# Optimization experiments

Hardware: AMD Instinct MI355X
Metric: run time of the kernel (lower is better)

The kernel has to match this reference:

```python
import jax, jax.numpy as jnp
import numpy as np

EMB = 512
HEADS = 8

def setup_inputs() -> dict:
    key = jax.random.key(0)
    ks = jax.random.split(key, 9)
    s = 1.0 / np.sqrt(EMB)
    return {
        'x':  jax.random.normal(ks[0], (4, 2048, EMB), dtype=jnp.float32),
        'Wq': jax.random.uniform(ks[1], (EMB, EMB), jnp.float32, -s, s),
        'bq': jax.random.uniform(ks[2], (EMB,), jnp.float32, -s, s),
        'Wk': jax.random.uniform(ks[3], (EMB, EMB), jnp.float32, -s, s),
        'bk': jax.random.uniform(ks[4], (EMB,), jnp.float32, -s, s),
        'Wv': jax.random.uniform(ks[5], (EMB, EMB), jnp.float32, -s, s),
        'bv': jax.random.uniform(ks[6], (EMB,), jnp.float32, -s, s),
        'Wo': jax.random.uniform(ks[7], (EMB, EMB), jnp.float32, -s, s),
        'bo': jax.random.uniform(ks[8], (EMB,), jnp.float32, -s, s),
    }

def reference(x, Wq, bq, Wk, bk, Wv, bv, Wo, bo):
    b, n, e = x.shape
    h = HEADS
    d = e // h
    def split_heads(t):
        return t.reshape(b, n, h, d).transpose(0, 2, 1, 3)  # b h n d
    q = split_heads(x @ Wq.T + bq)
    k = split_heads(x @ Wk.T + bk)
    v = split_heads(x @ Wv.T + bv)
    energy = jnp.einsum('bhqd,bhkd->bhqk', q, k)
    scaling = jnp.sqrt(jnp.float32(e))  # NOTE: sqrt(emb_size), not sqrt(head_dim), per source
    att = jax.nn.softmax(energy / scaling, axis=-1)
    out = jnp.einsum('bhal,bhlv->bhav', att, v)  # b h n d
    out = out.transpose(0, 2, 1, 3).reshape(b, n, e)
    return out @ Wo.T + bo
```

## Files before the change

kernel.cpp:

```cpp
#include <hip/hip_runtime.h>

typedef float f32x4 __attribute__((ext_vector_type(4)));
typedef float f32x16 __attribute__((ext_vector_type(16)));
typedef short bf16x8 __attribute__((ext_vector_type(8)));
typedef unsigned int uint;
typedef unsigned short ushort_t;

#define EMB    512
#define NSEQ   2048
#define NBATCH 4
#define NHEAD  8
#define MROWS  (NBATCH * NSEQ)
#define CEXP   0.06375872f

__device__ __forceinline__ uint f2bf(float x) {
    uint u = __builtin_bit_cast(uint, x);
    return (u + 0x7fffu + ((u >> 16) & 1u)) >> 16;
}

__device__ __forceinline__ void glds16(const void* g, void* l) {
    __builtin_amdgcn_global_load_lds(
        (const __attribute__((address_space(1))) uint*)g,
        (__attribute__((address_space(3))) uint*)l, 16, 0, 0);
}

__global__ __launch_bounds__(256)
void prep(const float* __restrict__ x,
          const float* __restrict__ Wq, const float* __restrict__ Wk,
          const float* __restrict__ Wv, const float* __restrict__ Wo,
          const float* __restrict__ bq, const float* __restrict__ bk,
          const float* __restrict__ bv,
          ushort_t* __restrict__ xb, ushort_t* __restrict__ Wqkvb,
          float* __restrict__ bqkv, ushort_t* __restrict__ Wob) {
    int t = blockIdx.x * 256 + threadIdx.x;
    {
        float4 v = ((const float4*)x)[t];
        uint2 p;
        p.x = f2bf(v.x) | (f2bf(v.y) << 16);
        p.y = f2bf(v.z) | (f2bf(v.w) << 16);
        ((uint2*)xb)[t] = p;
    }
    if (t < 65536) {
        float4 a = ((const float4*)Wq)[t];
        float4 b = ((const float4*)Wk)[t];
        float4 c = ((const float4*)Wv)[t];
        float4 d = ((const float4*)Wo)[t];
        uint2 p;
        p.x = f2bf(a.x) | (f2bf(a.y) << 16); p.y = f2bf(a.z) | (f2bf(a.w) << 16);
        ((uint2*)Wqkvb)[t] = p;
        p.x = f2bf(b.x) | (f2bf(b.y) << 16); p.y = f2bf(b.z) | (f2bf(b.w) << 16);
        ((uint2*)Wqkvb)[t + 65536] = p;
        p.x = f2bf(c.x) | (f2bf(c.y) << 16); p.y = f2bf(c.z) | (f2bf(c.w) << 16);
        ((uint2*)Wqkvb)[t + 131072] = p;
        p.x = f2bf(d.x) | (f2bf(d.y) << 16); p.y = f2bf(d.z) | (f2bf(d.w) << 16);
        ((uint2*)Wob)[t] = p;
    }
    if (t < 512) {
        bqkv[t] = bq[t]; bqkv[512 + t] = bk[t]; bqkv[1024 + t] = bv[t];
    }
}

template<int MODE>
__global__ __launch_bounds__(256)
void gemm128(const ushort_t* __restrict__ A, const ushort_t* __restrict__ BT,
             const float* __restrict__ bias, ushort_t* __restrict__ oQK,
             ushort_t* __restrict__ oVT, float* __restrict__ oC) {
    __shared__ ushort_t As[128][32];
    __shared__ ushort_t Bs[128][32];
    __shared__ float ep[32][132];
    const int tid = threadIdx.x, wave = tid >> 6, lane = tid & 63;
    const int m0 = blockIdx.x * 128, n0 = blockIdx.y * 128;
    const int wr = (wave & 1) * 64, wc = (wave >> 1) * 64;

    f32x4 acc[4][4];
#pragma unroll
    for (int i = 0; i < 4; ++i)
#pragma unroll
        for (int j = 0; j < 4; ++j) acc[i][j] = (f32x4){0.f, 0.f, 0.f, 0.f};

    const int grow = wave * 16 + (lane >> 2);
    const int gcol = (lane & 3) * 8;
    const ushort_t* Ag = A  + (size_t)(m0 + grow) * 512 + gcol;
    const ushort_t* Bg = BT + (size_t)(n0 + grow) * 512 + gcol;
    ushort_t* lA0 = &As[wave * 16][0];
    ushort_t* lA1 = &As[64 + wave * 16][0];
    ushort_t* lB0 = &Bs[wave * 16][0];
    ushort_t* lB1 = &Bs[64 + wave * 16][0];
    const int fr = lane & 15, fc = (lane >> 4) * 8;

    for (int kt = 0; kt < 16; ++kt) {
        __syncthreads();
        glds16(Ag + kt * 32,             lA0);
        glds16(Ag + kt * 32 + 64 * 512,  lA1);
        glds16(Bg + kt * 32,             lB0);
        glds16(Bg + kt * 32 + 64 * 512,  lB1);
        __syncthreads();
        bf16x8 af[4], bf[4];
#pragma unroll
        for (int i = 0; i < 4; ++i) af[i] = *(const bf16x8*)&As[wr + i * 16 + fr][fc];
#pragma unroll
        for (int j = 0; j < 4; ++j) bf[j] = *(const bf16x8*)&Bs[wc + j * 16 + fr][fc];
#pragma unroll
        for (int i = 0; i < 4; ++i)
#pragma unroll
            for (int j = 0; j < 4; ++j)
                acc[i][j] = __builtin_amdgcn_mfma_f32_16x16x32_bf16(af[i], bf[j], acc[i][j], 0, 0, 0);
    }

    const int col_l = lane & 15, row_l = (lane >> 4) * 4;

    if (MODE == 0 && n0 >= 1024) {
#pragma unroll
        for (int j = 0; j < 4; ++j) {
            const int col = n0 + wc + j * 16 + col_l;
            const float bv = bias[col];
#pragma unroll
            for (int i = 0; i < 4; ++i) {
                const int row = m0 + wr + i * 16 + row_l;
                f32x4 v = acc[i][j];
                v += (f32x4){bv, bv, bv, bv};
                const int e = col - 1024;
                const int b = row >> 11, tok = row & 2047;
                uint2 p;
                p.x = f2bf(v[0]) | (f2bf(v[1]) << 16);
                p.y = f2bf(v[2]) | (f2bf(v[3]) << 16);
                *(uint2*)&oVT[((size_t)(b * 512 + e)) * 2048 + tok] = p;
            }
        }
        return;
    }

    const float scale = (MODE == 0 && n0 < 512) ? CEXP : 1.0f;
    float bv[4];
#pragma unroll
    for (int j = 0; j < 4; ++j) bv[j] = bias[n0 + wc + j * 16 + col_l];

    const int erow = tid >> 3, eseg = (tid & 7) * 16;
#pragma unroll
    for (int c = 0; c < 4; ++c) {
        __syncthreads();
        if (wr == (c >> 1) * 64) {
#pragma unroll
            for (int ii = 0; ii < 2; ++ii) {
                const int i = (c & 1) * 2 + ii;
#pragma unroll
                for (int j = 0; j < 4; ++j) {
                    f32x4 v = acc[i][j];
#pragma unroll
                    for (int r = 0; r < 4; ++r)
                        ep[ii * 16 + row_l + r][wc + j * 16 + col_l] = (v[r] + bv[j]) * scale;
                }
            }
        }
        __syncthreads();
        const int grow2 = m0 + c * 32 + erow;
        if (MODE == 0) {
            uint4 o0, o1;
#pragma unroll
            for (int k = 0; k < 4; ++k) {
                uint lo = f2bf(ep[erow][eseg + k * 2])     | (f2bf(ep[erow][eseg + k * 2 + 1]) << 16);
                uint hi = f2bf(ep[erow][eseg + 8 + k * 2]) | (f2bf(ep[erow][eseg + 9 + k * 2]) << 16);
                ((uint*)&o0)[k] = lo; ((uint*)&o1)[k] = hi;
            }
            *(uint4*)&oQK[(size_t)grow2 * 1024 + n0 + eseg]     = o0;
            *(uint4*)&oQK[(size_t)grow2 * 1024 + n0 + eseg + 8] = o1;
        } else {
#pragma unroll
            for (int k = 0; k < 4; ++k) {
                f32x4 v = *(const f32x4*)&ep[erow][eseg + k * 4];
                *(f32x4*)&oC[(size_t)grow2 * 512 + n0 + eseg + k * 4] = v;
            }
        }
    }
}

template<int NSLICE>
__global__ __launch_bounds__(256, 4)
void attn_mfma(const ushort_t* __restrict__ QK, const ushort_t* __restrict__ VT,
               float* __restrict__ Op, float* __restrict__ Lp,
               ushort_t* __restrict__ AO) {
    __shared__ ushort_t Ks[64][72];
    __shared__ ushort_t Vs[64][72];

    const int tid = threadIdx.x, w = tid >> 6, lane = tid & 63;
    const int qt = blockIdx.x, bh = blockIdx.y, b = bh >> 3, h = bh & 7;
    const int slice = (NSLICE > 1) ? blockIdx.z : 0;
    const int l31 = lane & 31, lhi = lane >> 5;

    const int tok = qt * 128 + w * 32 + l31;
    const size_t qrow = (size_t)(b * NSEQ + tok);
    bf16x8 qf[4];
#pragma unroll
    for (int ks = 0; ks < 4; ++ks)
        qf[ks] = *(const bf16x8*)&QK[qrow * 1024 + h * 64 + ks * 16 + lhi * 8];

    f32x16 accO[2];
#pragma unroll
    for (int i = 0; i < 16; ++i) { accO[0][i] = 0.f; accO[1][i] = 0.f; }
    float lpart = 0.f;

    const int sr = tid & 63, sc = (tid >> 6) * 16;
    const ushort_t* Kg = QK + (size_t)(b * NSEQ) * 1024 + 512 + h * 64;
    const ushort_t* Vg = VT + ((size_t)(b * 512 + h * 64)) * 2048;

    const int kt0 = slice * (32 / NSLICE), kt1 = kt0 + 32 / NSLICE;
    for (int kt = kt0; kt < kt1; ++kt) {
        const int k0 = kt * 64;
        uint4 kv0 = *(const uint4*)&Kg[(size_t)(k0 + sr) * 1024 + sc];
        uint4 kv1 = *(const uint4*)&Kg[(size_t)(k0 + sr) * 1024 + sc + 8];
        uint4 vv0 = *(const uint4*)&Vg[(size_t)sr * 2048 + k0 + sc];
        uint4 vv1 = *(const uint4*)&Vg[(size_t)sr * 2048 + k0 + sc + 8];
        __syncthreads();
        *(uint4*)&Ks[sr][sc] = kv0;  *(uint4*)&Ks[sr][sc + 8] = kv1;
        *(uint4*)&Vs[sr][sc] = vv0;  *(uint4*)&Vs[sr][sc + 8] = vv1;
        __syncthreads();

#pragma unroll
        for (int ms = 0; ms < 2; ++ms) {
            f32x16 st;
#pragma unroll
            for (int i = 0; i < 16; ++i) st[i] = 0.f;
#pragma unroll
            for (int ks = 0; ks < 4; ++ks) {
                bf16x8 ka = *(const bf16x8*)&Ks[ms * 32 + l31][ks * 16 + lhi * 8];
                st = __builtin_amdgcn_mfma_f32_32x32x16_bf16(ka, qf[ks], st, 0, 0, 0);
            }
            uint dd[8], ee[8];
#pragma unroll
            for (int i = 0; i < 8; ++i) {
                uint ua = __builtin_bit_cast(uint, __builtin_amdgcn_exp2f(st[2 * i]));
                uint ub = __builtin_bit_cast(uint, __builtin_amdgcn_exp2f(st[2 * i + 1]));
                lpart += __builtin_bit_cast(float, ua & 0xffff0000u)
                       + __builtin_bit_cast(float, ub & 0xffff0000u);
                dd[i] = (ua >> 16) | (ub & 0xffff0000u);
            }
#pragma unroll
            for (int i = 0; i < 8; ++i) ee[i] = (uint)__shfl_xor((int)dd[i], 32);
#pragma unroll
            for (int s = 0; s < 2; ++s) {
                union { uint u[4]; bf16x8 v; } B;
                B.u[0] = lhi ? ee[4 * s + 2] : dd[4 * s + 0];
                B.u[1] = lhi ? ee[4 * s + 3] : dd[4 * s + 1];
                B.u[2] = lhi ? dd[4 * s + 2] : ee[4 * s + 0];
                B.u[3] = lhi ? dd[4 * s + 3] : ee[4 * s + 1];
                const int step = ms * 2 + s;
                bf16x8 va0 = *(const bf16x8*)&Vs[l31][step * 16 + lhi * 8];
                bf16x8 va1 = *(const bf16x8*)&Vs[32 + l31][step * 16 + lhi * 8];
                accO[0] = __builtin_amdgcn_mfma_f32_32x32x16_bf16(va0, B.v, accO[0], 0, 0, 0);
                accO[1] = __builtin_amdgcn_mfma_f32_32x32x16_bf16(va1, B.v, accO[1], 0, 0, 0);
            }
        }
    }

    const float lfull = lpart + __shfl_xor(lpart, 32);

    if (NSLICE == 1) {
        const float inv = 1.0f / lfull;
#pragma unroll
        for (int hf = 0; hf < 2; ++hf)
#pragma unroll
            for (int r = 0; r < 16; ++r) {
                const int d = (r & 3) + 8 * (r >> 2) + 4 * lhi + 32 * hf;
                AO[((size_t)(b * NSEQ + tok)) * 512 + h * 64 + d] =
                    (ushort_t)f2bf(accO[hf][r] * inv);
            }
    } else {
        if (lane < 32) Lp[(size_t)slice * 65536 + bh * 2048 + tok] = lfull;
        float* Os = Op + (size_t)slice * 4194304;
#pragma unroll
        for (int hf = 0; hf < 2; ++hf)
#pragma unroll
            for (int r = 0; r < 16; ++r) {
                const int d = (r & 3) + 8 * (r >> 2) + 4 * lhi + 32 * hf;
                Os[((size_t)(bh * 64 + d)) * 2048 + tok] = accO[hf][r];
            }
    }
}

__global__ __launch_bounds__(256)
void combine2T(const float* __restrict__ Op, const float* __restrict__ Lp,
               ushort_t* __restrict__ AO) {
    __shared__ float T[64][68];
    const int tid = threadIdx.x;
    const int tc = blockIdx.x, bh = blockIdx.y;
    const int b = bh >> 3, h = bh & 7;
    const int tok0 = tc * 64;

    const int d = tid >> 2, ts = (tid & 3) * 16;
    const float* P0 = Op + ((size_t)(bh * 64 + d)) * 2048 + tok0 + ts;
    const float* P1 = P0 + 4194304;
#pragma unroll
    for (int k = 0; k < 4; ++k) {
        f32x4 a = *(const f32x4*)(P0 + 4 * k);
        f32x4 c = *(const f32x4*)(P1 + 4 * k);
        *(f32x4*)&T[d][ts + 4 * k] = a + c;
    }
    __syncthreads();

    const int tk = tid >> 2, ds = (tid & 3) * 16;
    const int tok = tok0 + tk;
    const float inv = 1.0f / (Lp[bh * 2048 + tok] + Lp[65536 + bh * 2048 + tok]);
    uint o[8];
#pragma unroll
    for (int k = 0; k < 8; ++k) {
        float a = T[ds + 2 * k][tk] * inv;
        float c = T[ds + 2 * k + 1][tk] * inv;
        o[k] = f2bf(a) | (f2bf(c) << 16);
    }
    ushort_t* dst = AO + ((size_t)(b * NSEQ + tok)) * 512 + h * 64 + ds;
    *(uint4*)dst       = *(const uint4*)&o[0];
    *(uint4*)(dst + 8) = *(const uint4*)&o[4];
}

extern "C" void kernel_launch(void* const* d_in, const int* in_sizes, int n_in,
                              void* d_out, int out_size, void* d_ws, size_t ws_size,
                              hipStream_t stream) {
    const float* x  = (const float*)d_in[0];
    const float* Wq = (const float*)d_in[1];
    const float* bq = (const float*)d_in[2];
    const float* Wk = (const float*)d_in[3];
    const float* bk = (const float*)d_in[4];
    const float* Wv = (const float*)d_in[5];
    const float* bv = (const float*)d_in[6];
    const float* Wo = (const float*)d_in[7];
    const float* bo = (const float*)d_in[8];

    char* ws = (char*)d_ws;
    ushort_t* xb    = (ushort_t*)(ws);
    ushort_t* Wqkvb = (ushort_t*)(ws + 8388608);
    ushort_t* Wob   = (ushort_t*)(ws + 9961472);
    float*    bqkv  = (float*)   (ws + 10485760);
    ushort_t* QKb   = (ushort_t*)(ws + 10491904);
    ushort_t* VTg   = (ushort_t*)(ws + 27269120);
    ushort_t* AOb   = (ushort_t*)(ws + 35657728);
    float*    Opart = (float*)   (ws + 44046336);
    float*    Lpart = (float*)   (ws + 77600768);
    const bool split = ws_size >= 78125056;

    prep<<<4096, 256, 0, stream>>>(x, Wq, Wk, Wv, Wo, bq, bk, bv,
                                   xb, Wqkvb, bqkv, Wob);
    gemm128<0><<<dim3(64, 12), 256, 0, stream>>>(xb, Wqkvb, bqkv, QKb, VTg, nullptr);
    if (split) {
        attn_mfma<2><<<dim3(16, 32, 2), 256, 0, stream>>>(QKb, VTg, Opart, Lpart, nullptr);
        combine2T<<<dim3(32, 32), 256, 0, stream>>>(Opart, Lpart, AOb);
    } else {
        attn_mfma<1><<<dim3(16, 32, 1), 256, 0, stream>>>(QKb, VTg, nullptr, nullptr, AOb);
    }
    gemm128<1><<<dim3(64, 4), 256, 0, stream>>>(AOb, Wob, bo, nullptr, nullptr, (float*)d_out);
}
```

Baseline: 187.5 us.

## Split attention keys into four slices with bf16 partials and four-way combine

Raises the key-dimension split of the attention kernel from two slices to four, launching twice as many blocks for better occupancy across CUs. Partial outputs are stored as bf16 instead of fp32, so four slices take the same workspace as two fp32 slices did and combine traffic stays bounded. The combine kernel now sums four bf16 partials and four row-sum values. Row sums are placed at the start of the workspace, overlapping the x bf16 buffer, which is no longer needed at that point. Rounding the partials to bf16 adds some error before normalization.

After: 187.5 us. Within noise of the previous version (-0.0%).

```diff
diff --git a/kernel.cpp b/kernel.cpp
--- a/kernel.cpp
+++ b/kernel.cpp
@@ -177,7 +177,7 @@
 template<int NSLICE>
 __global__ __launch_bounds__(256, 4)
 void attn_mfma(const ushort_t* __restrict__ QK, const ushort_t* __restrict__ VT,
-               float* __restrict__ Op, float* __restrict__ Lp,
+               ushort_t* __restrict__ Op, float* __restrict__ Lp,
                ushort_t* __restrict__ AO) {
     __shared__ ushort_t Ks[64][72];
     __shared__ ushort_t Vs[64][72];
@@ -266,19 +266,19 @@
             }
     } else {
         if (lane < 32) Lp[(size_t)slice * 65536 + bh * 2048 + tok] = lfull;
-        float* Os = Op + (size_t)slice * 4194304;
+        ushort_t* Os = Op + (size_t)slice * 4194304;
 #pragma unroll
         for (int hf = 0; hf < 2; ++hf)
 #pragma unroll
             for (int r = 0; r < 16; ++r) {
                 const int d = (r & 3) + 8 * (r >> 2) + 4 * lhi + 32 * hf;
-                Os[((size_t)(bh * 64 + d)) * 2048 + tok] = accO[hf][r];
+                Os[((size_t)(bh * 64 + d)) * 2048 + tok] = (ushort_t)f2bf(accO[hf][r]);
             }
     }
 }
 
 __global__ __launch_bounds__(256)
-void combine2T(const float* __restrict__ Op, const float* __restrict__ Lp,
+void combine4T(const ushort_t* __restrict__ Op, const float* __restrict__ Lp,
                ushort_t* __restrict__ AO) {
     __shared__ float T[64][68];
     const int tid = threadIdx.x;
@@ -287,19 +287,34 @@
     const int tok0 = tc * 64;
 
     const int d = tid >> 2, ts = (tid & 3) * 16;
-    const float* P0 = Op + ((size_t)(bh * 64 + d)) * 2048 + tok0 + ts;
-    const float* P1 = P0 + 4194304;
-#pragma unroll
-    for (int k = 0; k < 4; ++k) {
-        f32x4 a = *(const f32x4*)(P0 + 4 * k);
-        f32x4 c = *(const f32x4*)(P1 + 4 * k);
-        *(f32x4*)&T[d][ts + 4 * k] = a + c;
-    }
+    float acc[16];
+#pragma unroll
+    for (int i = 0; i < 16; ++i) acc[i] = 0.f;
+#pragma unroll
+    for (int s = 0; s < 4; ++s) {
+        const ushort_t* P = Op + (size_t)s * 4194304
+                               + ((size_t)(bh * 64 + d)) * 2048 + tok0 + ts;
+#pragma unroll
+        for (int k2 = 0; k2 < 2; ++k2) {
+            uint4 u = *(const uint4*)(P + 8 * k2);
+#pragma unroll
+            for (int j = 0; j < 4; ++j) {
+                uint uw = ((const uint*)&u)[j];
+                acc[k2 * 8 + 2 * j]     += __builtin_bit_cast(float, uw << 16);
+                acc[k2 * 8 + 2 * j + 1] += __builtin_bit_cast(float, uw & 0xffff0000u);
+            }
+        }
+    }
+#pragma unroll
+    for (int k = 0; k < 4; ++k)
+        *(f32x4*)&T[d][ts + 4 * k] = *(const f32x4*)&acc[4 * k];
     __syncthreads();
 
     const int tk = tid >> 2, ds = (tid & 3) * 16;
     const int tok = tok0 + tk;
-    const float inv = 1.0f / (Lp[bh * 2048 + tok] + Lp[65536 + bh * 2048 + tok]);
+    const float l = Lp[bh * 2048 + tok]           + Lp[65536 + bh * 2048 + tok]
+                  + Lp[131072 + bh * 2048 + tok]  + Lp[196608 + bh * 2048 + tok];
+    const float inv = 1.0f / l;
     uint o[8];
 #pragma unroll
     for (int k = 0; k < 8; ++k) {
@@ -333,16 +348,16 @@
     ushort_t* QKb   = (ushort_t*)(ws + 10491904);
     ushort_t* VTg   = (ushort_t*)(ws + 27269120);
     ushort_t* AOb   = (ushort_t*)(ws + 35657728);
-    float*    Opart = (float*)   (ws + 44046336);
-    float*    Lpart = (float*)   (ws + 77600768);
+    ushort_t* Opart = (ushort_t*)(ws + 44046336);
+    float*    Lpart = (float*)   (ws);
     const bool split = ws_size >= 78125056;
 
     prep<<<4096, 256, 0, stream>>>(x, Wq, Wk, Wv, Wo, bq, bk, bv,
                                    xb, Wqkvb, bqkv, Wob);
     gemm128<0><<<dim3(64, 12), 256, 0, stream>>>(xb, Wqkvb, bqkv, QKb, VTg, nullptr);
     if (split) {
-        attn_mfma<2><<<dim3(16, 32, 2), 256, 0, stream>>>(QKb, VTg, Opart, Lpart, nullptr);
-        combine2T<<<dim3(32, 32), 256, 0, stream>>>(Opart, Lpart, AOb);
+        attn_mfma<4><<<dim3(16, 32, 4), 256, 0, stream>>>(QKb, VTg, Opart, Lpart, nullptr);
+        combine4T<<<dim3(32, 32), 256, 0, stream>>>(Opart, Lpart, AOb);
     } else {
         attn_mfma<1><<<dim3(16, 32, 1), 256, 0, stream>>>(QKb, VTg, nullptr, nullptr, AOb);
     }
```
